# Optimization experiments

Measured on AMD Instinct MI355X. Metric: run time of the kernel, lower is better.

## Reference

```python
import jax, jax.numpy as jnp
import numpy as np

EPS = 1e-5

def conv3d(x, w, b):
    y = jax.lax.conv_general_dilated(x, w, (1, 1, 1), [(1, 1), (1, 1), (1, 1)],
                                     dimension_numbers=('NCDHW', 'OIDHW', 'NCDHW'))
    return y + b[None, :, None, None, None]

def batchnorm(x, g, b):
    # training-mode BN: biased batch statistics over (N, D, H, W)
    m = jnp.mean(x, axis=(0, 2, 3, 4), keepdims=True)
    v = jnp.mean((x - m) ** 2, axis=(0, 2, 3, 4), keepdims=True)
    return (x - m) * jax.lax.rsqrt(v + EPS) * g[None, :, None, None, None] + b[None, :, None, None, None]

def deform_conv3d(x, offset, w, b):
    # x: (B,C,D,H,W); offset: (B, 3*27, D,H,W); w: (O,C,3,3,3)
    B, C, D, H, W = x.shape
    N = 27
    xp = jnp.pad(x, ((0, 0), (0, 0), (1, 1), (1, 1), (1, 1)))
    Dp, Hp, Wp = D + 2, H + 2, W + 2
    off = offset.reshape(B, 3, N, D, H, W)
    kk = jnp.arange(3, dtype=x.dtype) - 1.0  # kernel taps -1,0,1
    kd, kh, kw = [a.reshape(-1) for a in jnp.meshgrid(kk, kk, kk, indexing='ij')]
    # sampling positions in padded coords: p0 (=out idx + pad) + kernel tap + learned offset
    pd = jnp.clip((jnp.arange(D, dtype=x.dtype) + 1.0)[None, None, :, None, None]
                  + kd[None, :, None, None, None] + off[:, 0], 0.0, Dp - 1)
    ph = jnp.clip((jnp.arange(H, dtype=x.dtype) + 1.0)[None, None, None, :, None]
                  + kh[None, :, None, None, None] + off[:, 1], 0.0, Hp - 1)
    pw = jnp.clip((jnp.arange(W, dtype=x.dtype) + 1.0)[None, None, None, None, :]
                  + kw[None, :, None, None, None] + off[:, 2], 0.0, Wp - 1)
    q0d = jnp.clip(jnp.floor(pd), 0, Dp - 2); td = jnp.clip(pd - q0d, 0.0, 1.0)
    q0h = jnp.clip(jnp.floor(ph), 0, Hp - 2); th = jnp.clip(ph - q0h, 0.0, 1.0)
    q0w = jnp.clip(jnp.floor(pw), 0, Wp - 2); tw = jnp.clip(pw - q0w, 0.0, 1.0)
    q0d = q0d.astype(jnp.int32); q0h = q0h.astype(jnp.int32); q0w = q0w.astype(jnp.int32)
    xf = xp.reshape(B, C, -1)
    acc = jnp.zeros((B, C, N, D, H, W), dtype=x.dtype)
    for i in (0, 1):
        for j in (0, 1):
            for k in (0, 1):
                idx = ((q0d + i) * Hp + (q0h + j)) * Wp + (q0w + k)  # (B,N,D,H,W)
                g = ((td if i else 1.0 - td) * (th if j else 1.0 - th) * (tw if k else 1.0 - tw))
                gath = jnp.take_along_axis(xf, idx.reshape(B, 1, -1), axis=2).reshape(B, C, N, D, H, W)
                acc = acc + g[:, None] * gath
    out = jnp.einsum('bcndhw,ocn->bodhw', acc, w.reshape(w.shape[0], C, N))
    return out + b[None, :, None, None, None]


def setup_inputs() -> dict:
    ks = jax.random.split(jax.random.key(0), 16)
    s = 0.05
    f32 = jnp.float32
    return {
        'x': jax.random.normal(ks[0], (4, 1, 28, 28, 8), f32),
        'c1w': jax.random.normal(ks[1], (32, 1, 3, 3, 3), f32) * s, 'c1b': jnp.zeros((32,), f32),
        'g1': jnp.ones((32,), f32), 'b1': jnp.zeros((32,), f32),
        'c2w': jax.random.normal(ks[2], (64, 32, 3, 3, 3), f32) * s, 'c2b': jnp.zeros((64,), f32),
        'g2': jnp.ones((64,), f32), 'b2': jnp.zeros((64,), f32),
        'c3w': jax.random.normal(ks[3], (128, 64, 3, 3, 3), f32) * s, 'c3b': jnp.zeros((128,), f32),
        'g3': jnp.ones((128,), f32), 'b3': jnp.zeros((128,), f32),
        'ow': jax.random.normal(ks[4], (81, 128, 3, 3, 3), f32) * s, 'ob': jnp.zeros((81,), f32),
        'dw': jax.random.normal(ks[5], (128, 128, 3, 3, 3), f32) * s, 'db': jnp.zeros((128,), f32),
        'g4': jnp.ones((128,), f32), 'b4': jnp.zeros((128,), f32),
        'fcw': jax.random.normal(ks[6], (10, 128), f32) * s, 'fcb': jnp.zeros((10,), f32),
    }


def reference(x, c1w, c1b, g1, b1, c2w, c2b, g2, b2, c3w, c3b, g3, b3,
              ow, ob, dw, db, g4, b4, fcw, fcb):
    h = batchnorm(jax.nn.relu(conv3d(x, c1w, c1b)), g1, b1)
    h = batchnorm(jax.nn.relu(conv3d(h, c2w, c2b)), g2, b2)
    h = batchnorm(jax.nn.relu(conv3d(h, c3w, c3b)), g3, b3)
    offsets = conv3d(h, ow, ob)
    h = batchnorm(jax.nn.relu(deform_conv3d(h, offsets, dw, db)), g4, b4)
    pooled = jnp.mean(h, axis=(2, 3, 4))  # avg_pool over full (28,28,d) extent
    logits = pooled @ fcw.T + fcb
    return jax.nn.log_softmax(logits, axis=1), offsets
```

## Files before the change

kernel.cpp:

```cpp
#include <hip/hip_runtime.h>
#include <hip/hip_bf16.h>
#include <math.h>

#define BB 4
#define SP 6272
#define NSP 25088
#define EPS 1e-5f

typedef unsigned short u16;
typedef __attribute__((ext_vector_type(8))) short v8s;
typedef __attribute__((ext_vector_type(4))) float v4f;

__device__ __forceinline__ u16 f2b(float f) {
    unsigned u = __float_as_uint(f);
    return (u16)((u + 0x7fffu + ((u >> 16) & 1u)) >> 16);
}
__device__ __forceinline__ float b2f(u16 s) {
    return __uint_as_float(((unsigned)s) << 16);
}
__device__ __forceinline__ float b2f_lo(unsigned x) { return __uint_as_float(x << 16); }
__device__ __forceinline__ float b2f_hi(unsigned x) { return __uint_as_float(x & 0xffff0000u); }
__device__ __forceinline__ unsigned pk2(float a, float b) {
    __hip_bfloat162 h = __float22bfloat162_rn(make_float2(a, b));
    unsigned u;
    __builtin_memcpy(&u, &h, 4);
    return u;
}

__global__ __launch_bounds__(256) __attribute__((amdgpu_waves_per_eu(1, 4)))
void conv1_shfl(const float* __restrict__ X, const float* __restrict__ Wt,
                const float* __restrict__ bias, u16* __restrict__ Ybf,
                float* __restrict__ s_sum, float* __restrict__ s_sq)
{
    const int OT = 16;
    __shared__ float red[4][32];
    int xblk = blockIdx.x;
    int sblk = (xblk & 7) * 13 + (xblk >> 3);
    if (sblk >= 98) return;
    int t = threadIdx.x;
    int s = sblk * 256 + t;
    int b = s / SP;
    int sp = s - b * SP;
    int d = sp / 224;
    int r = sp - d * 224;
    int h = r >> 3;
    int w = r & 7;
    int o0 = blockIdx.y * OT;

    float mdh[9]; int odh[9];
    #pragma unroll
    for (int i = 0; i < 3; i++) {
        int dd = d + i - 1;
        float md = ((unsigned)dd < 28u) ? 1.f : 0.f;
        int ddc = min(max(dd, 0), 27);
        #pragma unroll
        for (int j = 0; j < 3; j++) {
            int hh = h + j - 1;
            float mh = ((unsigned)hh < 28u) ? 1.f : 0.f;
            int hhc = min(max(hh, 0), 27);
            mdh[i * 3 + j] = md * mh;
            odh[i * 3 + j] = ddc * 224 + hhc * 8 + w;
        }
    }
    float mw0 = (w > 0) ? 1.f : 0.f;
    float mw2 = (w < 7) ? 1.f : 0.f;

    float acc[OT];
    #pragma unroll
    for (int oo = 0; oo < OT; oo++) acc[oo] = bias[o0 + oo];

    const float* xc = X + (size_t)b * SP;
    #pragma unroll
    for (int t9 = 0; t9 < 9; t9++) {
        float x0 = xc[odh[t9]];
        float m = mdh[t9];
        float xm = __shfl_up(x0, 1, 64) * (m * mw0);
        float xz = x0 * m;
        float xp = __shfl_down(x0, 1, 64) * (m * mw2);
        #pragma unroll
        for (int oo = 0; oo < OT; oo++) {
            const float* wp = Wt + (size_t)(o0 + oo) * 27 + t9 * 3;
            acc[oo] = fmaf(xm, wp[0], acc[oo]);
            acc[oo] = fmaf(xz, wp[1], acc[oo]);
            acc[oo] = fmaf(xp, wp[2], acc[oo]);
        }
    }
    float sv[OT];
    #pragma unroll
    for (int oo = 0; oo < OT; oo++) sv[oo] = fmaxf(acc[oo], 0.f);

    unsigned pk[8];
    #pragma unroll
    for (int j = 0; j < 8; j++) pk[j] = pk2(sv[2 * j], sv[2 * j + 1]);
    u16* row = Ybf + (size_t)(b * SP + sp) * 32 + o0;
    *(uint4*)(row)     = make_uint4(pk[0], pk[1], pk[2], pk[3]);
    *(uint4*)(row + 8) = make_uint4(pk[4], pk[5], pk[6], pk[7]);

    int l = t & 63, wvv = t >> 6;
    #pragma unroll
    for (int oo = 0; oo < OT; oo++) {
        float ss = sv[oo], qv = ss * ss;
        #pragma unroll
        for (int m = 1; m < 64; m <<= 1) {
            ss += __shfl_xor(ss, m, 64);
            qv += __shfl_xor(qv, m, 64);
        }
        if (l == 0) { red[wvv][oo] = ss; red[wvv][16 + oo] = qv; }
    }
    __syncthreads();
    if (t < 32) {
        float tot = red[0][t] + red[1][t] + red[2][t] + red[3][t];
        if (t < 16) atomicAdd(&s_sum[o0 + t], tot);
        else        atomicAdd(&s_sq[o0 + t - 16], tot);
    }
}

__global__ __launch_bounds__(256) void prepack_all(const float* __restrict__ c2w,
        const float* __restrict__ c3w, const float* __restrict__ ow,
        const float* __restrict__ dw, u16* __restrict__ wpk2,
        u16* __restrict__ wpk3, u16* __restrict__ wpko, u16* __restrict__ dwa,
        float* __restrict__ ws0)
{
    int bx = blockIdx.x;
    if (bx >= 4536) {
        int i = (bx - 4536) * 256 + threadIdx.x;
        if (i < 2048) ws0[i] = 0.f;
        return;
    }
    int idx = bx * 256 + threadIdx.x;
    if (idx < 55296) {
        int i = idx;
        int j = i & 7, r = (i >> 3) & 15, q = (i >> 7) & 3;
        int ot = (i >> 9) & 3, t = i >> 11;
        int o = ot * 16 + r, c = q * 8 + j;
        wpk2[i] = f2b(c2w[((size_t)o * 32 + c) * 27 + t]);
    } else if (idx < 276480) {
        int i = idx - 55296;
        int j = i & 7, r = (i >> 3) & 15, q = (i >> 7) & 3;
        int ch = (i >> 9) & 1, ot = (i >> 10) & 7, t = i >> 13;
        int o = ot * 16 + r, c = ch * 32 + q * 8 + j;
        wpk3[i] = f2b(c3w[((size_t)o * 64 + c) * 27 + t]);
    } else if (idx < 718848) {
        int i = idx - 276480;
        int j = i & 7, r = (i >> 3) & 15, q = (i >> 7) & 3;
        int ch = (i >> 9) & 3, ot = (i >> 11) & 7, t = i >> 14;
        int o = ot * 16 + r, c = ch * 32 + q * 8 + j;
        wpko[i] = f2b((o < 81) ? ow[((size_t)o * 128 + c) * 27 + t] : 0.f);
    } else {
        int i = idx - 718848;
        int j = i & 7, r = (i >> 3) & 15, q = (i >> 7) & 3;
        int kc = (i >> 9) & 3, ot = (i >> 11) & 7, n = i >> 14;
        int o = ot * 16 + r, c = kc * 32 + q * 8 + j;
        dwa[i] = f2b(dw[((size_t)o * 128 + c) * 27 + n]);
    }
}

template<int CIN, int OPAD, bool OFFOUT, bool BNIN, bool WIDE>
__global__ __launch_bounds__(256) __attribute__((amdgpu_waves_per_eu(1, 4)))
void conv_mfma(const u16* __restrict__ X, const u16* __restrict__ Wpk,
               const float* __restrict__ bias, u16* __restrict__ Ybf,
               float* __restrict__ offs, float* __restrict__ s_sum,
               float* __restrict__ s_sq, const float* __restrict__ in_sum,
               const float* __restrict__ in_sq, const float* __restrict__ in_g,
               const float* __restrict__ in_b)
{
    const int HS = CIN + 8;
    const int NOT = OPAD / 16;
    const int NC = CIN / 32;
    __shared__ u16 xs[160 * HS];
    __shared__ float scin[BNIN ? CIN : 1], shin[BNIN ? CIN : 1];

    int tid = threadIdx.x;
    int fid = blockIdx.x;
    int g = (fid & 7) * 98 + (fid >> 3);
    int b = g / 196;
    int rem = g - b * 196;
    int d0 = (rem / 14) * 2, h0 = (rem % 14) * 2;

    if (BNIN) {
        if (tid < CIN) {
            float m = in_sum[tid] * (1.f / NSP);
            float v = in_sq[tid] * (1.f / NSP) - m * m;
            float sc = in_g[tid] * rsqrtf(v + EPS);
            scin[tid] = sc;
            shin[tid] = in_b[tid] - m * sc;
        }
        __syncthreads();
    }

    const int NCH = CIN / 8;
    for (int idx = tid; idx < 160 * NCH; idx += 256) {
        int pos = idx / NCH, ch = idx - pos * NCH;
        int dz = pos / 40, r2 = pos - dz * 40;
        int hz = r2 / 10, wz = r2 - hz * 10;
        int dd = d0 + dz - 1, hh = h0 + hz - 1, ww = wz - 1;
        uint4 val = make_uint4(0, 0, 0, 0);
        if ((unsigned)dd < 28u && (unsigned)hh < 28u && (unsigned)ww < 8u) {
            val = *(const uint4*)(X + ((size_t)(b * SP + dd * 224 + hh * 8 + ww) * CIN + ch * 8));
            if (BNIN) {
                int cb = ch * 8;
                float f0 = b2f_lo(val.x) * scin[cb]     + shin[cb];
                float f1 = b2f_hi(val.x) * scin[cb + 1] + shin[cb + 1];
                float f2 = b2f_lo(val.y) * scin[cb + 2] + shin[cb + 2];
                float f3 = b2f_hi(val.y) * scin[cb + 3] + shin[cb + 3];
                float f4 = b2f_lo(val.z) * scin[cb + 4] + shin[cb + 4];
                float f5 = b2f_hi(val.z) * scin[cb + 5] + shin[cb + 5];
                float f6 = b2f_lo(val.w) * scin[cb + 6] + shin[cb + 6];
                float f7 = b2f_hi(val.w) * scin[cb + 7] + shin[cb + 7];
                val.x = pk2(f0, f1); val.y = pk2(f2, f3);
                val.z = pk2(f4, f5); val.w = pk2(f6, f7);
            }
        }
        *(uint4*)(xs + pos * HS + ch * 8) = val;
    }
    __syncthreads();

    int l = tid & 63, wv = tid >> 6;
    int q = l >> 4, r = l & 15;
    int hl = r >> 3, wl = r & 7;

    if (OFFOUT) {
        int dl = wv >> 1;
        int ot0 = (wv & 1) * 3;
        const u16* ap = xs + ((4 + hl + 1) * 10 + wl + 1) * HS + 8 * q + dl * 40 * HS;
        v4f acc[3];
        acc[0] = (v4f){0.f,0.f,0.f,0.f};
        acc[1] = (v4f){0.f,0.f,0.f,0.f};
        acc[2] = (v4f){0.f,0.f,0.f,0.f};
        #pragma unroll
        for (int t = 0; t < 27; t++) {
            const int koff = ((t / 9) - 1) * 40 + (((t / 3) % 3) - 1) * 10 + (t % 3) - 1;
            const u16* wt = Wpk + ((size_t)(t * NOT + ot0) * NC << 9) + l * 8;
            #pragma unroll
            for (int ch = 0; ch < NC; ch++) {
                v8s a0 = *(const v8s*)(ap + koff * HS + ch * 32);
                v8s b0 = *(const v8s*)(wt + ch * 512);
                v8s b1 = *(const v8s*)(wt + (NC + ch) * 512);
                v8s b2 = *(const v8s*)(wt + (2 * NC + ch) * 512);
                acc[0] = __builtin_amdgcn_mfma_f32_16x16x32_bf16(a0, b0, acc[0], 0, 0, 0);
                acc[1] = __builtin_amdgcn_mfma_f32_16x16x32_bf16(a0, b1, acc[1], 0, 0, 0);
// ... 54 lines not shown
                for (int rg = 0; rg < 4; rg++) {
                    int rowl = q * 4 + rg;
                    int sp = (d0 + s2) * 224 + (h0 + (rowl >> 3)) * 8 + (rowl & 7);
                    float v = fmaxf(A[rg] + bo, 0.f);
                    Ybf[(size_t)(b * SP + sp) * OPAD + oo] = f2b(v);
                    rs += v; rq += v * v;
                }
            }
            rs += __shfl_xor(rs, 16, 64); rs += __shfl_xor(rs, 32, 64);
            rq += __shfl_xor(rq, 16, 64); rq += __shfl_xor(rq, 32, 64);
            if (l < 16) { atomicAdd(&s_sum[o_base + l], rs); atomicAdd(&s_sq[o_base + l], rq); }
        }
        return;
    }

    int o_base = blockIdx.y * 64 + wv * 16;
    int o = o_base + r;
    int otg = o_base >> 4;

    v4f acc0 = {0.f, 0.f, 0.f, 0.f}, acc1 = {0.f, 0.f, 0.f, 0.f};
    #pragma unroll
    for (int t = 0; t < 27; t++) {
        const int koff = ((t / 9) - 1) * 40 + (((t / 3) % 3) - 1) * 10 + (t % 3) - 1;
        const u16* wt = Wpk + ((size_t)(t * NOT + otg) * NC << 9) + l * 8;
        #pragma unroll
        for (int ch = 0; ch < NC; ch++) {
            v8s a0 = *(const v8s*)(a0p + koff * HS + ch * 32);
            v8s a1 = *(const v8s*)(a1p + koff * HS + ch * 32);
            v8s bf = *(const v8s*)(wt + ch * 512);
            acc0 = __builtin_amdgcn_mfma_f32_16x16x32_bf16(a0, bf, acc0, 0, 0, 0);
            acc1 = __builtin_amdgcn_mfma_f32_16x16x32_bf16(a1, bf, acc1, 0, 0, 0);
        }
    }

    {
        float bo = bias[o];
        float rs = 0.f, rq = 0.f;
        #pragma unroll
        for (int s2 = 0; s2 < 2; s2++) {
            v4f A = s2 ? acc1 : acc0;
            #pragma unroll
            for (int rg = 0; rg < 4; rg++) {
                int rowl = q * 4 + rg;
                int sp = (d0 + s2) * 224 + (h0 + (rowl >> 3)) * 8 + (rowl & 7);
                float v = fmaxf(A[rg] + bo, 0.f);
                Ybf[(size_t)(b * SP + sp) * OPAD + o] = f2b(v);
                rs += v; rq += v * v;
            }
        }
        rs += __shfl_xor(rs, 16, 64); rs += __shfl_xor(rs, 32, 64);
        rq += __shfl_xor(rq, 16, 64); rq += __shfl_xor(rq, 32, 64);
        if (l < 16) { atomicAdd(&s_sum[o_base + l], rs); atomicAdd(&s_sq[o_base + l], rq); }
    }
}

template<int C>
__global__ __launch_bounds__(256) void bn_bf(const u16* __restrict__ Y,
        const float* __restrict__ s_sum, const float* __restrict__ s_sq,
        const float* __restrict__ g, const float* __restrict__ bb,
        u16* __restrict__ Xo)
{
    __shared__ float sc_s[C], sh_s[C];
    int t = threadIdx.x;
    if (t < C) {
        float m  = s_sum[t] * (1.f / NSP);
        float v  = s_sq[t] * (1.f / NSP) - m * m;
        float sc = g[t] * rsqrtf(v + EPS);
        sc_s[t] = sc;
        sh_s[t] = bb[t] - m * sc;
    }
    __syncthreads();
    int idx = blockIdx.x * 256 + t;
    uint4 v = ((const uint4*)Y)[idx];
    int cb = (idx & (C / 8 - 1)) * 8;
    float f0 = b2f_lo(v.x) * sc_s[cb]     + sh_s[cb];
    float f1 = b2f_hi(v.x) * sc_s[cb + 1] + sh_s[cb + 1];
    float f2 = b2f_lo(v.y) * sc_s[cb + 2] + sh_s[cb + 2];
    float f3 = b2f_hi(v.y) * sc_s[cb + 3] + sh_s[cb + 3];
    float f4 = b2f_lo(v.z) * sc_s[cb + 4] + sh_s[cb + 4];
    float f5 = b2f_hi(v.z) * sc_s[cb + 5] + sh_s[cb + 5];
    float f6 = b2f_lo(v.w) * sc_s[cb + 6] + sh_s[cb + 6];
    float f7 = b2f_hi(v.w) * sc_s[cb + 7] + sh_s[cb + 7];
    uint4 pk;
    pk.x = pk2(f0, f1); pk.y = pk2(f2, f3);
    pk.z = pk2(f4, f5); pk.w = pk2(f6, f7);
    ((uint4*)Xo)[idx] = pk;
}

__global__ __launch_bounds__(256) __attribute__((amdgpu_waves_per_eu(1, 4)))
void deform_pool(const u16* __restrict__ Ht, const float* __restrict__ OFF,
                 const u16* __restrict__ Wa, const float* __restrict__ db,
                 float* __restrict__ pooledraw, float* __restrict__ sumsq4)
{
    __shared__ float offs_lds[81 * 32];
    __shared__ int ig_s[2][32][8][2];
    __shared__ u16 Vb[2][32][136];
    __shared__ float reds[128], redq[128];

    int fid = blockIdx.x;
    int xcd = fid & 7;
    int local = fid >> 3;
    if (local >= 98) return;
    int b = xcd >> 1;
    int d = (xcd & 1) * 14 + local / 7;
    int h0 = (local % 7) * 4;

    int t = threadIdx.x;
    if (t < 128) { reds[t] = 0.f; redq[t] = 0.f; }

    int gp = t >> 3, gcr = t & 7;
    int glh = gp >> 3, gw = gp & 7, gh = h0 + glh;
    int co = t & 15, pg = t >> 4;
    int l = t & 63, wv = t >> 6;
    int q = l >> 4, r = l & 15;

    v4f acc[2][2];
    acc[0][0] = (v4f){0.f,0.f,0.f,0.f}; acc[0][1] = (v4f){0.f,0.f,0.f,0.f};
    acc[1][0] = (v4f){0.f,0.f,0.f,0.f}; acc[1][1] = (v4f){0.f,0.f,0.f,0.f};

    const u16* hb = Ht + (size_t)b * SP * 128;

    for (int i = t; i < 2592; i += 256) {
        int ch = i >> 5, p = i & 31;
        offs_lds[i] = OFF[(size_t)b * 81 * SP + (size_t)ch * SP
                          + d * 224 + (h0 + (p >> 3)) * 8 + (p & 7)];
    }

    auto GEOM = [&](int n, int tap) {
        int kd = n / 9 - 1, kh = (n / 3) % 3 - 1, kw = n % 3 - 1;
        float od  = offs_lds[n * 32 + gp];
        float oh  = offs_lds[(27 + n) * 32 + gp];
        float owv = offs_lds[(54 + n) * 32 + gp];
        float pd = fminf(fmaxf((float)(d + 1 + kd) + od, 0.f), 29.f);
        float ph = fminf(fmaxf((float)(gh + 1 + kh) + oh, 0.f), 29.f);
        float pw = fminf(fmaxf((float)(gw + 1 + kw) + owv, 0.f), 9.f);
        float qd = fminf(floorf(pd), 28.f);
        float qh = fminf(floorf(ph), 28.f);
        float qw = fminf(floorf(pw), 8.f);
        float td = fminf(pd - qd, 1.f);
        float th = fminf(ph - qh, 1.f);
        float tw = fminf(pw - qw, 1.f);
        int iqd = (int)qd - 1, iqh = (int)qh - 1, iqw = (int)qw - 1;
        int i = gcr >> 2, j = (gcr >> 1) & 1, k = gcr & 1;
        int du = iqd + i, hu = iqh + j, wu = iqw + k;
        bool val = (unsigned)du < 28u && (unsigned)hu < 28u && (unsigned)wu < 8u;
        float gg = (i ? td : 1.f - td) * (j ? th : 1.f - th) * (k ? tw : 1.f - tw);
        ig_s[tap][gp][gcr][0] = val ? (du * 224 + hu * 8 + wu) : 0;
        ig_s[tap][gp][gcr][1] = __float_as_int(val ? gg : 0.f);
    };

    auto SAMPLE = [&](int tap) {
        #pragma unroll
        for (int pp = 0; pp < 2; pp++) {
            int p = pg * 2 + pp;
            float va[8] = {0.f,0.f,0.f,0.f,0.f,0.f,0.f,0.f};
            #pragma unroll
            for (int cr = 0; cr < 8; cr++) {
                int2 pr = *(const int2*)&ig_s[tap][p][cr][0];
                float gg = __int_as_float(pr.y);
                uint4 xv = *(const uint4*)(hb + (size_t)pr.x * 128 + co * 8);
                va[0] = fmaf(gg, b2f_lo(xv.x), va[0]);
                va[1] = fmaf(gg, b2f_hi(xv.x), va[1]);
                va[2] = fmaf(gg, b2f_lo(xv.y), va[2]);
                va[3] = fmaf(gg, b2f_hi(xv.y), va[3]);
                va[4] = fmaf(gg, b2f_lo(xv.z), va[4]);
                va[5] = fmaf(gg, b2f_hi(xv.z), va[5]);
                va[6] = fmaf(gg, b2f_lo(xv.w), va[6]);
                va[7] = fmaf(gg, b2f_hi(xv.w), va[7]);
            }
            uint4 pk;
            pk.x = pk2(va[0], va[1]); pk.y = pk2(va[2], va[3]);
            pk.z = pk2(va[4], va[5]); pk.w = pk2(va[6], va[7]);
            *(uint4*)&Vb[tap][p][co * 8] = pk;
        }
    };

    auto MFMA_TAP = [&](int n, int tap) {
        const u16* wn = Wa + (size_t)n * 16384;
        #pragma unroll
        for (int oti = 0; oti < 2; oti++) {
            int ot = wv * 2 + oti;
            #pragma unroll
            for (int kc = 0; kc < 4; kc++) {
                v8s af = *(const v8s*)(wn + ((((ot * 4 + kc) * 4 + q) * 16 + r) * 8));
                v8s bf0 = *(const v8s*)&Vb[tap][r][kc * 32 + q * 8];
                v8s bf1 = *(const v8s*)&Vb[tap][16 + r][kc * 32 + q * 8];
                acc[oti][0] = __builtin_amdgcn_mfma_f32_16x16x32_bf16(af, bf0, acc[oti][0], 0, 0, 0);
                acc[oti][1] = __builtin_amdgcn_mfma_f32_16x16x32_bf16(af, bf1, acc[oti][1], 0, 0, 0);
            }
        }
    };

    for (int it = 0; it < 14; it++) {
        int n0 = it * 2, n1 = n0 + 1;
        bool two = (n1 < 27);
        __syncthreads();
        GEOM(n0, 0);
        if (two) GEOM(n1, 1);
        __syncthreads();
        SAMPLE(0);
        if (two) SAMPLE(1);
        __syncthreads();
        MFMA_TAP(n0, 0);
        if (two) MFMA_TAP(n1, 1);
    }

    #pragma unroll
    for (int oti = 0; oti < 2; oti++) {
        #pragma unroll
        for (int rg = 0; rg < 4; rg++) {
            int o = (wv * 2 + oti) * 16 + q * 4 + rg;
            float bo = db[o];
            float v0 = fmaxf(acc[oti][0][rg] + bo, 0.f);
            float v1 = fmaxf(acc[oti][1][rg] + bo, 0.f);
            float s = v0 + v1, qq = v0 * v0 + v1 * v1;
            s += __shfl_xor(s, 1, 64);  qq += __shfl_xor(qq, 1, 64);
            s += __shfl_xor(s, 2, 64);  qq += __shfl_xor(qq, 2, 64);
            s += __shfl_xor(s, 4, 64);  qq += __shfl_xor(qq, 4, 64);
            s += __shfl_xor(s, 8, 64);  qq += __shfl_xor(qq, 8, 64);
            if (r == 0) { atomicAdd(&reds[o], s); atomicAdd(&redq[o], qq); }
        }
    }
    __syncthreads();
    if (t < 128) {
        atomicAdd(&pooledraw[b * 128 + t], reds[t]);
        atomicAdd(&sumsq4[t], redq[t]);
    }
}

__global__ __launch_bounds__(256) void final_head_emit(const float* __restrict__ pooledraw,
        const float* __restrict__ sumsq4, const float* __restrict__ g4,
        const float* __restrict__ b4, const float* __restrict__ fcw,
        const float* __restrict__ fcb, float* __restrict__ out)
{
    int t = threadIdx.x;
    __shared__ float pooled_s[4][128];
    __shared__ float logits[4][10];
    if (t < 128) {
        float s0 = pooledraw[t], s1 = pooledraw[128 + t];
        float s2 = pooledraw[256 + t], s3 = pooledraw[384 + t];
        float tot = s0 + s1 + s2 + s3;
        float m  = tot * (1.f / NSP);
        float v  = sumsq4[t] * (1.f / NSP) - m * m;
        float sc = g4[t] * rsqrtf(v + EPS);
        float sh = b4[t] - m * sc;
        pooled_s[0][t] = s0 * (1.f / SP) * sc + sh;
        pooled_s[1][t] = s1 * (1.f / SP) * sc + sh;
        pooled_s[2][t] = s2 * (1.f / SP) * sc + sh;
        pooled_s[3][t] = s3 * (1.f / SP) * sc + sh;
    }
    __syncthreads();
    if (t < 40) {
        int b = t / 10, j = t % 10;
        float l = fcb[j];
        for (int c = 0; c < 128; c++) l = fmaf(pooled_s[b][c], fcw[j * 128 + c], l);
        logits[b][j] = l;
    }
    __syncthreads();
    if (t < 4) {
        float mx = -1e30f;
        for (int j = 0; j < 10; j++) mx = fmaxf(mx, logits[t][j]);
        float se = 0.f;
        for (int j = 0; j < 10; j++) se += expf(logits[t][j] - mx);
        float lse = mx + logf(se);
        for (int j = 0; j < 10; j++) out[t * 10 + j] = logits[t][j] - lse;
    }
}

extern "C" void kernel_launch(void* const* d_in, const int* in_sizes, int n_in,
                              void* d_out, int out_size, void* d_ws, size_t ws_size,
                              hipStream_t stream)
{
    (void)in_sizes; (void)n_in; (void)out_size; (void)ws_size;
    const float* x   = (const float*)d_in[0];
    const float* c1w = (const float*)d_in[1];
    const float* c1b = (const float*)d_in[2];
    const float* g1  = (const float*)d_in[3];
    const float* b1  = (const float*)d_in[4];
    const float* c2w = (const float*)d_in[5];
    const float* c2b = (const float*)d_in[6];
    const float* g2  = (const float*)d_in[7];
    const float* b2  = (const float*)d_in[8];
    const float* c3w = (const float*)d_in[9];
    const float* c3b = (const float*)d_in[10];
    const float* g3  = (const float*)d_in[11];
    const float* b3  = (const float*)d_in[12];
    const float* ow  = (const float*)d_in[13];
    const float* ob  = (const float*)d_in[14];
    const float* dw  = (const float*)d_in[15];
    const float* db  = (const float*)d_in[16];
    const float* g4  = (const float*)d_in[17];
    const float* b4  = (const float*)d_in[18];
    const float* fcw = (const float*)d_in[19];
    const float* fcb = (const float*)d_in[20];

    float* ws = (float*)d_ws;
    float* S1 = ws + 0,   *Q1 = ws + 32;
    float* S2 = ws + 64,  *Q2 = ws + 128;
    float* S3 = ws + 192, *Q3 = ws + 320;
    float* PO = ws + 448;
    float* Q4 = ws + 960;
    u16* y1bf = (u16*)(ws + 2048);
    u16* y2bf = y1bf + 802816;
    u16* y3bf = y2bf + 1605632;
    u16* x3bf = y3bf + 3211264;
    u16* wpk2 = x3bf + 3211264;
    u16* wpk3 = wpk2 + 55296;
    u16* wpko = wpk3 + 221184;
    u16* dwa  = wpko + 442368;

    float* outf = (float*)d_out;
    float* offp = outf + 40;

    prepack_all<<<4544, 256, 0, stream>>>(c2w, c3w, ow, dw, wpk2, wpk3, wpko, dwa, ws);

    conv1_shfl<<<dim3(104, 2), 256, 0, stream>>>(x, c1w, c1b, y1bf, S1, Q1);

    conv_mfma<32, 64, false, true, false><<<dim3(784, 1), 256, 0, stream>>>(
        y1bf, wpk2, c2b, y2bf, nullptr, S2, Q2, S1, Q1, g1, b1);

    conv_mfma<64, 128, false, true, true><<<dim3(784, 1), 256, 0, stream>>>(
        y2bf, wpk3, c3b, y3bf, nullptr, S3, Q3, S2, Q2, g2, b2);

    bn_bf<128><<<1568, 256, 0, stream>>>(y3bf, S3, Q3, g3, b3, x3bf);

    conv_mfma<128, 128, true, false, false><<<dim3(784, 1), 256, 0, stream>>>(
        x3bf, wpko, ob, nullptr, offp, nullptr, nullptr, nullptr, nullptr, nullptr, nullptr);

    deform_pool<<<800, 256, 0, stream>>>(x3bf, offp, dwa, db, PO, Q4);
    final_head_emit<<<1, 256, 0, stream>>>(PO, Q4, g4, b4, fcw, fcb, outf);
}
```

Measured before the change: 339.6 us.

## Fuse final head into deform_pool via last-block counter; batch gather loads

Folds the final BN/FC/log-softmax kernel into deform_pool. Each block bumps a global atomic counter, and the last block to finish reads the accumulated sums and computes the head, which removes one kernel launch. It also restructures SAMPLE to issue all eight gather loads before the FMAs and to use packed float2 math, aiming for more memory-level parallelism. The counter at ws+1100 must be zeroed before each call (possibly in prepack, not visible here), and the restructuring adds register pressure.

```diff
diff --git a/kernel.cpp b/kernel.cpp
--- a/kernel.cpp
+++ b/kernel.cpp
@@ -10,6 +10,7 @@
 typedef unsigned short u16;
 typedef __attribute__((ext_vector_type(8))) short v8s;
 typedef __attribute__((ext_vector_type(4))) float v4f;
+typedef __attribute__((ext_vector_type(2))) float f32x2;
 
 __device__ __forceinline__ u16 f2b(float f) {
     unsigned u = __float_as_uint(f);
@@ -384,180 +385,199 @@
 __global__ __launch_bounds__(256) __attribute__((amdgpu_waves_per_eu(1, 4)))
 void deform_pool(const u16* __restrict__ Ht, const float* __restrict__ OFF,
                  const u16* __restrict__ Wa, const float* __restrict__ db,
-                 float* __restrict__ pooledraw, float* __restrict__ sumsq4)
+                 float* __restrict__ pooledraw, float* __restrict__ sumsq4,
+                 unsigned* __restrict__ cnt, const float* __restrict__ g4,
+                 const float* __restrict__ b4, const float* __restrict__ fcw,
+                 const float* __restrict__ fcb, float* __restrict__ out)
 {
     __shared__ float offs_lds[81 * 32];
     __shared__ int ig_s[2][32][8][2];
     __shared__ u16 Vb[2][32][136];
     __shared__ float reds[128], redq[128];
+    __shared__ unsigned done_s;
 
     int fid = blockIdx.x;
     int xcd = fid & 7;
     int local = fid >> 3;
-    if (local >= 98) return;
-    int b = xcd >> 1;
-    int d = (xcd & 1) * 14 + local / 7;
-    int h0 = (local % 7) * 4;
-
     int t = threadIdx.x;
-    if (t < 128) { reds[t] = 0.f; redq[t] = 0.f; }
-
-    int gp = t >> 3, gcr = t & 7;
-    int glh = gp >> 3, gw = gp & 7, gh = h0 + glh;
-    int co = t & 15, pg = t >> 4;
-    int l = t & 63, wv = t >> 6;
-    int q = l >> 4, r = l & 15;
-
-    v4f acc[2][2];
-    acc[0][0] = (v4f){0.f,0.f,0.f,0.f}; acc[0][1] = (v4f){0.f,0.f,0.f,0.f};
-    acc[1][0] = (v4f){0.f,0.f,0.f,0.f}; acc[1][1] = (v4f){0.f,0.f,0.f,0.f};
-
-    const u16* hb = Ht + (size_t)b * SP * 128;
-
-    for (int i = t; i < 2592; i += 256) {
-        int ch = i >> 5, p = i & 31;
-        offs_lds[i] = OFF[(size_t)b * 81 * SP + (size_t)ch * SP
-                          + d * 224 + (h0 + (p >> 3)) * 8 + (p & 7)];
-    }
-
-    auto GEOM = [&](int n, int tap) {
-        int kd = n / 9 - 1, kh = (n / 3) % 3 - 1, kw = n % 3 - 1;
-        float od  = offs_lds[n * 32 + gp];
-        float oh  = offs_lds[(27 + n) * 32 + gp];
-        float owv = offs_lds[(54 + n) * 32 + gp];
-        float pd = fminf(fmaxf((float)(d + 1 + kd) + od, 0.f), 29.f);
-        float ph = fminf(fmaxf((float)(gh + 1 + kh) + oh, 0.f), 29.f);
-        float pw = fminf(fmaxf((float)(gw + 1 + kw) + owv, 0.f), 9.f);
-        float qd = fminf(floorf(pd), 28.f);
-        float qh = fminf(floorf(ph), 28.f);
-        float qw = fminf(floorf(pw), 8.f);
-        float td = fminf(pd - qd, 1.f);
-        float th = fminf(ph - qh, 1.f);
-        float tw = fminf(pw - qw, 1.f);
-        int iqd = (int)qd - 1, iqh = (int)qh - 1, iqw = (int)qw - 1;
-        int i = gcr >> 2, j = (gcr >> 1) & 1, k = gcr & 1;
-        int du = iqd + i, hu = iqh + j, wu = iqw + k;
-        bool val = (unsigned)du < 28u && (unsigned)hu < 28u && (unsigned)wu < 8u;
-        float gg = (i ? td : 1.f - td) * (j ? th : 1.f - th) * (k ? tw : 1.f - tw);
-        ig_s[tap][gp][gcr][0] = val ? (du * 224 + hu * 8 + wu) : 0;
-        ig_s[tap][gp][gcr][1] = __float_as_int(val ? gg : 0.f);
-    };
-
-    auto SAMPLE = [&](int tap) {
-        #pragma unroll
-        for (int pp = 0; pp < 2; pp++) {
-            int p = pg * 2 + pp;
-            float va[8] = {0.f,0.f,0.f,0.f,0.f,0.f,0.f,0.f};
+
+    if (local < 98) {
+        int b = xcd >> 1;
+        int d = (xcd & 1) * 14 + local / 7;
+        int h0 = (local % 7) * 4;
+
+        if (t < 128) { reds[t] = 0.f; redq[t] = 0.f; }
+
+        int gp = t >> 3, gcr = t & 7;
+        int glh = gp >> 3, gw = gp & 7, gh = h0 + glh;
+        int co = t & 15, pg = t >> 4;
+        int l = t & 63, wv = t >> 6;
+        int q = l >> 4, r = l & 15;
+
+        v4f acc[2][2];
+        acc[0][0] = (v4f){0.f,0.f,0.f,0.f}; acc[0][1] = (v4f){0.f,0.f,0.f,0.f};
+        acc[1][0] = (v4f){0.f,0.f,0.f,0.f}; acc[1][1] = (v4f){0.f,0.f,0.f,0.f};
+
+        const u16* hb = Ht + (size_t)b * SP * 128;
+
+        for (int i = t; i < 2592; i += 256) {
+            int ch = i >> 5, p = i & 31;
+            offs_lds[i] = OFF[(size_t)b * 81 * SP + (size_t)ch * SP
+                              + d * 224 + (h0 + (p >> 3)) * 8 + (p & 7)];
+        }
+
+        auto GEOM = [&](int n, int tap) {
+            int kd = n / 9 - 1, kh = (n / 3) % 3 - 1, kw = n % 3 - 1;
+            float od  = offs_lds[n * 32 + gp];
+            float oh  = offs_lds[(27 + n) * 32 + gp];
+            float owv = offs_lds[(54 + n) * 32 + gp];
+            float pd = fminf(fmaxf((float)(d + 1 + kd) + od, 0.f), 29.f);
+            float ph = fminf(fmaxf((float)(gh + 1 + kh) + oh, 0.f), 29.f);
+            float pw = fminf(fmaxf((float)(gw + 1 + kw) + owv, 0.f), 9.f);
+            float qd = fminf(floorf(pd), 28.f);
+            float qh = fminf(floorf(ph), 28.f);
+            float qw = fminf(floorf(pw), 8.f);
+            float td = fminf(pd - qd, 1.f);
+            float th = fminf(ph - qh, 1.f);
+            float tw = fminf(pw - qw, 1.f);
+            int iqd = (int)qd - 1, iqh = (int)qh - 1, iqw = (int)qw - 1;
+            int i = gcr >> 2, j = (gcr >> 1) & 1, k = gcr & 1;
+            int du = iqd + i, hu = iqh + j, wu = iqw + k;
+            bool val = (unsigned)du < 28u && (unsigned)hu < 28u && (unsigned)wu < 8u;
+            float gg = (i ? td : 1.f - td) * (j ? th : 1.f - th) * (k ? tw : 1.f - tw);
+            ig_s[tap][gp][gcr][0] = val ? (du * 224 + hu * 8 + wu) : 0;
+            ig_s[tap][gp][gcr][1] = __float_as_int(val ? gg : 0.f);
+        };
+
+        auto SAMPLE = [&](int tap) {
             #pragma unroll
-            for (int cr = 0; cr < 8; cr++) {
-                int2 pr = *(const int2*)&ig_s[tap][p][cr][0];
-                float gg = __int_as_float(pr.y);
-                uint4 xv = *(const uint4*)(hb + (size_t)pr.x * 128 + co * 8);
-                va[0] = fmaf(gg, b2f_lo(xv.x), va[0]);
-                va[1] = fmaf(gg, b2f_hi(xv.x), va[1]);
-                va[2] = fmaf(gg, b2f_lo(xv.y), va[2]);
-                va[3] = fmaf(gg, b2f_hi(xv.y), va[3]);
-                va[4] = fmaf(gg, b2f_lo(xv.z), va[4]);
-                va[5] = fmaf(gg, b2f_hi(xv.z), va[5]);
-                va[6] = fmaf(gg, b2f_lo(xv.w), va[6]);
-                va[7] = fmaf(gg, b2f_hi(xv.w), va[7]);
-            }
-            uint4 pk;
-            pk.x = pk2(va[0], va[1]); pk.y = pk2(va[2], va[3]);
-            pk.z = pk2(va[4], va[5]); pk.w = pk2(va[6], va[7]);
-            *(uint4*)&Vb[tap][p][co * 8] = pk;
-        }
-    };
-
-    auto MFMA_TAP = [&](int n, int tap) {
-        const u16* wn = Wa + (size_t)n * 16384;
+            for (int pp = 0; pp < 2; pp++) {
+                int p = pg * 2 + pp;
+                int2 prs[8];
+                #pragma unroll
+                for (int cr = 0; cr < 8; cr++)
+                    prs[cr] = *(const int2*)&ig_s[tap][p][cr][0];
+                uint4 xv[8];
+                #pragma unroll
+                for (int cr = 0; cr < 8; cr++)
+                    xv[cr] = *(const uint4*)(hb + (size_t)prs[cr].x * 128 + co * 8);
+                f32x2 va2[4];
+                va2[0] = (f32x2){0.f, 0.f}; va2[1] = (f32x2){0.f, 0.f};
+                va2[2] = (f32x2){0.f, 0.f}; va2[3] = (f32x2){0.f, 0.f};
+                #pragma unroll
+                for (int cr = 0; cr < 8; cr++) {
+                    float gg = __int_as_float(prs[cr].y);
+                    f32x2 g2 = {gg, gg};
+                    f32x2 x0 = { b2f_lo(xv[cr].x), b2f_hi(xv[cr].x) };
+                    f32x2 x1 = { b2f_lo(xv[cr].y), b2f_hi(xv[cr].y) };
+                    f32x2 x2 = { b2f_lo(xv[cr].z), b2f_hi(xv[cr].z) };
+                    f32x2 x3 = { b2f_lo(xv[cr].w), b2f_hi(xv[cr].w) };
+                    va2[0] = g2 * x0 + va2[0];
+                    va2[1] = g2 * x1 + va2[1];
+                    va2[2] = g2 * x2 + va2[2];
+                    va2[3] = g2 * x3 + va2[3];
+                }
+                uint4 pk;
+                pk.x = pk2(va2[0].x, va2[0].y); pk.y = pk2(va2[1].x, va2[1].y);
+                pk.z = pk2(va2[2].x, va2[2].y); pk.w = pk2(va2[3].x, va2[3].y);
+                *(uint4*)&Vb[tap][p][co * 8] = pk;
+            }
+        };
+
+        auto MFMA_TAP = [&](int n, int tap) {
+            const u16* wn = Wa + (size_t)n * 16384;
+            #pragma unroll
+            for (int oti = 0; oti < 2; oti++) {
+                int ot = wv * 2 + oti;
+                #pragma unroll
+                for (int kc = 0; kc < 4; kc++) {
+                    v8s af = *(const v8s*)(wn + ((((ot * 4 + kc) * 4 + q) * 16 + r) * 8));
+                    v8s bf0 = *(const v8s*)&Vb[tap][r][kc * 32 + q * 8];
+                    v8s bf1 = *(const v8s*)&Vb[tap][16 + r][kc * 32 + q * 8];
+                    acc[oti][0] = __builtin_amdgcn_mfma_f32_16x16x32_bf16(af, bf0, acc[oti][0], 0, 0, 0);
+                    acc[oti][1] = __builtin_amdgcn_mfma_f32_16x16x32_bf16(af, bf1, acc[oti][1], 0, 0, 0);
+                }
+            }
+        };
+
+        for (int it = 0; it < 14; it++) {
+            int n0 = it * 2, n1 = n0 + 1;
+            bool two = (n1 < 27);
+            __syncthreads();
+            GEOM(n0, 0);
+            if (two) GEOM(n1, 1);
+            __syncthreads();
+            SAMPLE(0);
+            if (two) SAMPLE(1);
+            __syncthreads();
+            MFMA_TAP(n0, 0);
+            if (two) MFMA_TAP(n1, 1);
+        }
+
         #pragma unroll
         for (int oti = 0; oti < 2; oti++) {
-            int ot = wv * 2 + oti;
             #pragma unroll
-            for (int kc = 0; kc < 4; kc++) {
-                v8s af = *(const v8s*)(wn + ((((ot * 4 + kc) * 4 + q) * 16 + r) * 8));
-                v8s bf0 = *(const v8s*)&Vb[tap][r][kc * 32 + q * 8];
-                v8s bf1 = *(const v8s*)&Vb[tap][16 + r][kc * 32 + q * 8];
-                acc[oti][0] = __builtin_amdgcn_mfma_f32_16x16x32_bf16(af, bf0, acc[oti][0], 0, 0, 0);
-                acc[oti][1] = __builtin_amdgcn_mfma_f32_16x16x32_bf16(af, bf1, acc[oti][1], 0, 0, 0);
-            }
-        }
-    };
-
-    for (int it = 0; it < 14; it++) {
-        int n0 = it * 2, n1 = n0 + 1;
-        bool two = (n1 < 27);
+            for (int rg = 0; rg < 4; rg++) {
+                int o = (wv * 2 + oti) * 16 + q * 4 + rg;
+                float bo = db[o];
+                float v0 = fmaxf(acc[oti][0][rg] + bo, 0.f);
+                float v1 = fmaxf(acc[oti][1][rg] + bo, 0.f);
+                float s = v0 + v1, qq = v0 * v0 + v1 * v1;
+                s += __shfl_xor(s, 1, 64);  qq += __shfl_xor(qq, 1, 64);
+                s += __shfl_xor(s, 2, 64);  qq += __shfl_xor(qq, 2, 64);
+                s += __shfl_xor(s, 4, 64);  qq += __shfl_xor(qq, 4, 64);
+                s += __shfl_xor(s, 8, 64);  qq += __shfl_xor(qq, 8, 64);
+                if (r == 0) { atomicAdd(&reds[o], s); atomicAdd(&redq[o], qq); }
+            }
+        }
         __syncthreads();
-        GEOM(n0, 0);
-        if (two) GEOM(n1, 1);
+        if (t < 128) {
+            atomicAdd(&pooledraw[b * 128 + t], reds[t]);
+            atomicAdd(&sumsq4[t], redq[t]);
+        }
+    }
+
+    __syncthreads();
+    if (t == 0) {
+        __threadfence();
+        done_s = atomicAdd(cnt, 1u);
+    }
+    __syncthreads();
+    if (done_s == 799u) {
+        __shared__ float pooled_s[4][128];
+        __shared__ float logits_s[4][10];
+        if (t < 128) {
+            float s0 = __hip_atomic_load(&pooledraw[t],       __ATOMIC_RELAXED, __HIP_MEMORY_SCOPE_AGENT);
+            float s1 = __hip_atomic_load(&pooledraw[128 + t], __ATOMIC_RELAXED, __HIP_MEMORY_SCOPE_AGENT);
+            float s2 = __hip_atomic_load(&pooledraw[256 + t], __ATOMIC_RELAXED, __HIP_MEMORY_SCOPE_AGENT);
+            float s3 = __hip_atomic_load(&pooledraw[384 + t], __ATOMIC_RELAXED, __HIP_MEMORY_SCOPE_AGENT);
+            float qv = __hip_atomic_load(&sumsq4[t],          __ATOMIC_RELAXED, __HIP_MEMORY_SCOPE_AGENT);
+            float tot = s0 + s1 + s2 + s3;
+            float m  = tot * (1.f / NSP);
+            float v  = qv * (1.f / NSP) - m * m;
+            float sc = g4[t] * rsqrtf(v + EPS);
+            float sh = b4[t] - m * sc;
+            pooled_s[0][t] = s0 * (1.f / SP) * sc + sh;
+            pooled_s[1][t] = s1 * (1.f / SP) * sc + sh;
+            pooled_s[2][t] = s2 * (1.f / SP) * sc + sh;
+            pooled_s[3][t] = s3 * (1.f / SP) * sc + sh;
+        }
         __syncthreads();
-        SAMPLE(0);
-        if (two) SAMPLE(1);
+        if (t < 40) {
+            int b = t / 10, j = t % 10;
+            float lg = fcb[j];
+            for (int c = 0; c < 128; c++) lg = fmaf(pooled_s[b][c], fcw[j * 128 + c], lg);
+            logits_s[b][j] = lg;
+        }
         __syncthreads();
-        MFMA_TAP(n0, 0);
-        if (two) MFMA_TAP(n1, 1);
-    }
-
-    #pragma unroll
-    for (int oti = 0; oti < 2; oti++) {
-        #pragma unroll
-        for (int rg = 0; rg < 4; rg++) {
-            int o = (wv * 2 + oti) * 16 + q * 4 + rg;
-            float bo = db[o];
-            float v0 = fmaxf(acc[oti][0][rg] + bo, 0.f);
-            float v1 = fmaxf(acc[oti][1][rg] + bo, 0.f);
-            float s = v0 + v1, qq = v0 * v0 + v1 * v1;
-            s += __shfl_xor(s, 1, 64);  qq += __shfl_xor(qq, 1, 64);
-            s += __shfl_xor(s, 2, 64);  qq += __shfl_xor(qq, 2, 64);
-            s += __shfl_xor(s, 4, 64);  qq += __shfl_xor(qq, 4, 64);
-            s += __shfl_xor(s, 8, 64);  qq += __shfl_xor(qq, 8, 64);
-            if (r == 0) { atomicAdd(&reds[o], s); atomicAdd(&redq[o], qq); }
-        }
-    }
-    __syncthreads();
-    if (t < 128) {
-        atomicAdd(&pooledraw[b * 128 + t], reds[t]);
-        atomicAdd(&sumsq4[t], redq[t]);
-    }
-}
-
-__global__ __launch_bounds__(256) void final_head_emit(const float* __restrict__ pooledraw,
-        const float* __restrict__ sumsq4, const float* __restrict__ g4,
-        const float* __restrict__ b4, const float* __restrict__ fcw,
-        const float* __restrict__ fcb, float* __restrict__ out)
-{
-    int t = threadIdx.x;
-    __shared__ float pooled_s[4][128];
-    __shared__ float logits[4][10];
-    if (t < 128) {
-        float s0 = pooledraw[t], s1 = pooledraw[128 + t];
-        float s2 = pooledraw[256 + t], s3 = pooledraw[384 + t];
-        float tot = s0 + s1 + s2 + s3;
-        float m  = tot * (1.f / NSP);
-        float v  = sumsq4[t] * (1.f / NSP) - m * m;
-        float sc = g4[t] * rsqrtf(v + EPS);
-        float sh = b4[t] - m * sc;
-        pooled_s[0][t] = s0 * (1.f / SP) * sc + sh;
-        pooled_s[1][t] = s1 * (1.f / SP) * sc + sh;
-        pooled_s[2][t] = s2 * (1.f / SP) * sc + sh;
-        pooled_s[3][t] = s3 * (1.f / SP) * sc + sh;
-    }
-    __syncthreads();
-    if (t < 40) {
-        int b = t / 10, j = t % 10;
-        float l = fcb[j];
-        for (int c = 0; c < 128; c++) l = fmaf(pooled_s[b][c], fcw[j * 128 + c], l);
-        logits[b][j] = l;
-    }
-    __syncthreads();
-    if (t < 4) {
-        float mx = -1e30f;
-        for (int j = 0; j < 10; j++) mx = fmaxf(mx, logits[t][j]);
-        float se = 0.f;
-        for (int j = 0; j < 10; j++) se += expf(logits[t][j] - mx);
-        float lse = mx + logf(se);
-        for (int j = 0; j < 10; j++) out[t * 10 + j] = logits[t][j] - lse;
+        if (t < 4) {
+            float mx = -1e30f;
+            for (int j = 0; j < 10; j++) mx = fmaxf(mx, logits_s[t][j]);
+            float se = 0.f;
+            for (int j = 0; j < 10; j++) se += expf(logits_s[t][j] - mx);
+            float lse = mx + logf(se);
+            for (int j = 0; j < 10; j++) out[t * 10 + j] = logits_s[t][j] - lse;
+        }
     }
 }
 
@@ -594,6 +614,7 @@
     float* S3 = ws + 192, *Q3 = ws + 320;
     float* PO = ws + 448;
     float* Q4 = ws + 960;
+    unsigned* cnt = (unsigned*)(ws + 1100);
     u16* y1bf = (u16*)(ws + 2048);
     u16* y2bf = y1bf + 802816;
     u16* y3bf = y2bf + 1605632;
@@ -621,6 +642,6 @@
     conv_mfma<128, 128, true, false, false><<<dim3(784, 1), 256, 0, stream>>>(
         x3bf, wpko, ob, nullptr, offp, nullptr, nullptr, nullptr, nullptr, nullptr, nullptr);
 
-    deform_pool<<<800, 256, 0, stream>>>(x3bf, offp, dwa, db, PO, Q4);
-    final_head_emit<<<1, 256, 0, stream>>>(PO, Q4, g4, b4, fcw, fcb, outf);
-}
+    deform_pool<<<800, 256, 0, stream>>>(x3bf, offp, dwa, db, PO, Q4, cnt,
+                                         g4, b4, fcw, fcb, outf);
+}
```

New measurement: 343.2 us. No clear change (+1.0%).

## Fuse conv1 into prepack launch and BN3 into offset-conv input path

Applied to the files above, without the earlier changes.

Moves the conv1 computation into the prepack kernel as extra blocks and replaces its atomics with per-block partial sums, which conv2 reduces at startup. The offset conv now applies BN3 on the fly from the raw conv3 output, and extra blocks of the same launch write the normalized x3 buffer for the deform stage. Two kernel launches are removed, cutting launch overhead and one pass over memory, at the cost of redundant per-block stat reductions and mixed-role grids.

```diff
diff --git a/kernel.cpp b/kernel.cpp
--- a/kernel.cpp
+++ b/kernel.cpp
@@ -27,107 +27,109 @@
     return u;
 }
 
-__global__ __launch_bounds__(256) __attribute__((amdgpu_waves_per_eu(1, 4)))
-void conv1_shfl(const float* __restrict__ X, const float* __restrict__ Wt,
-                const float* __restrict__ bias, u16* __restrict__ Ybf,
-                float* __restrict__ s_sum, float* __restrict__ s_sq)
-{
-    const int OT = 16;
-    __shared__ float red[4][32];
-    int xblk = blockIdx.x;
-    int sblk = (xblk & 7) * 13 + (xblk >> 3);
-    if (sblk >= 98) return;
-    int t = threadIdx.x;
-    int s = sblk * 256 + t;
-    int b = s / SP;
-    int sp = s - b * SP;
-    int d = sp / 224;
-    int r = sp - d * 224;
-    int h = r >> 3;
-    int w = r & 7;
-    int o0 = blockIdx.y * OT;
-
-    float mdh[9]; int odh[9];
-    #pragma unroll
-    for (int i = 0; i < 3; i++) {
-        int dd = d + i - 1;
-        float md = ((unsigned)dd < 28u) ? 1.f : 0.f;
-        int ddc = min(max(dd, 0), 27);
-        #pragma unroll
-        for (int j = 0; j < 3; j++) {
-            int hh = h + j - 1;
-            float mh = ((unsigned)hh < 28u) ? 1.f : 0.f;
-            int hhc = min(max(hh, 0), 27);
-            mdh[i * 3 + j] = md * mh;
-            odh[i * 3 + j] = ddc * 224 + hhc * 8 + w;
-        }
-    }
-    float mw0 = (w > 0) ? 1.f : 0.f;
-    float mw2 = (w < 7) ? 1.f : 0.f;
-
-    float acc[OT];
-    #pragma unroll
-    for (int oo = 0; oo < OT; oo++) acc[oo] = bias[o0 + oo];
-
-    const float* xc = X + (size_t)b * SP;
-    #pragma unroll
-    for (int t9 = 0; t9 < 9; t9++) {
-        float x0 = xc[odh[t9]];
-        float m = mdh[t9];
-        float xm = __shfl_up(x0, 1, 64) * (m * mw0);
-        float xz = x0 * m;
-        float xp = __shfl_down(x0, 1, 64) * (m * mw2);
-        #pragma unroll
-        for (int oo = 0; oo < OT; oo++) {
-            const float* wp = Wt + (size_t)(o0 + oo) * 27 + t9 * 3;
-            acc[oo] = fmaf(xm, wp[0], acc[oo]);
-            acc[oo] = fmaf(xz, wp[1], acc[oo]);
-            acc[oo] = fmaf(xp, wp[2], acc[oo]);
-        }
-    }
-    float sv[OT];
-    #pragma unroll
-    for (int oo = 0; oo < OT; oo++) sv[oo] = fmaxf(acc[oo], 0.f);
-
-    unsigned pk[8];
-    #pragma unroll
-    for (int j = 0; j < 8; j++) pk[j] = pk2(sv[2 * j], sv[2 * j + 1]);
-    u16* row = Ybf + (size_t)(b * SP + sp) * 32 + o0;
-    *(uint4*)(row)     = make_uint4(pk[0], pk[1], pk[2], pk[3]);
-    *(uint4*)(row + 8) = make_uint4(pk[4], pk[5], pk[6], pk[7]);
-
-    int l = t & 63, wvv = t >> 6;
-    #pragma unroll
-    for (int oo = 0; oo < OT; oo++) {
-        float ss = sv[oo], qv = ss * ss;
-        #pragma unroll
-        for (int m = 1; m < 64; m <<= 1) {
-            ss += __shfl_xor(ss, m, 64);
-            qv += __shfl_xor(qv, m, 64);
-        }
-        if (l == 0) { red[wvv][oo] = ss; red[wvv][16 + oo] = qv; }
-    }
-    __syncthreads();
-    if (t < 32) {
-        float tot = red[0][t] + red[1][t] + red[2][t] + red[3][t];
-        if (t < 16) atomicAdd(&s_sum[o0 + t], tot);
-        else        atomicAdd(&s_sq[o0 + t - 16], tot);
-    }
-}
-
 __global__ __launch_bounds__(256) void prepack_all(const float* __restrict__ c2w,
         const float* __restrict__ c3w, const float* __restrict__ ow,
         const float* __restrict__ dw, u16* __restrict__ wpk2,
         u16* __restrict__ wpk3, u16* __restrict__ wpko, u16* __restrict__ dwa,
-        float* __restrict__ ws0)
+        float* __restrict__ ws0, const float* __restrict__ X,
+        const float* __restrict__ Wt, const float* __restrict__ c1b,
+        u16* __restrict__ Ybf, float* __restrict__ P1s, float* __restrict__ P1q)
 {
     int bx = blockIdx.x;
+    int tid = threadIdx.x;
+
+    if (bx >= 4544) {
+        const int OT = 16;
+        __shared__ float red[4][32];
+        int c = bx - 4544;
+        int xblk = c % 104;
+        int o0 = (c / 104) * OT;
+        int sblk = (xblk & 7) * 13 + (xblk >> 3);
+        if (sblk >= 98) return;
+        int t = tid;
+        int s = sblk * 256 + t;
+        int b = s / SP;
+        int sp = s - b * SP;
+        int d = sp / 224;
+        int r = sp - d * 224;
+        int h = r >> 3;
+        int w = r & 7;
+
+        float mdh[9]; int odh[9];
+        #pragma unroll
+        for (int i = 0; i < 3; i++) {
+            int dd = d + i - 1;
+            float md = ((unsigned)dd < 28u) ? 1.f : 0.f;
+            int ddc = min(max(dd, 0), 27);
+            #pragma unroll
+            for (int j = 0; j < 3; j++) {
+                int hh = h + j - 1;
+                float mh = ((unsigned)hh < 28u) ? 1.f : 0.f;
+                int hhc = min(max(hh, 0), 27);
+                mdh[i * 3 + j] = md * mh;
+                odh[i * 3 + j] = ddc * 224 + hhc * 8 + w;
+            }
+        }
+        float mw0 = (w > 0) ? 1.f : 0.f;
+        float mw2 = (w < 7) ? 1.f : 0.f;
+
+        float acc[OT];
+        #pragma unroll
+        for (int oo = 0; oo < OT; oo++) acc[oo] = c1b[o0 + oo];
+
+        const float* xc = X + (size_t)b * SP;
+        #pragma unroll
+        for (int t9 = 0; t9 < 9; t9++) {
+            float x0 = xc[odh[t9]];
+            float m = mdh[t9];
+            float xm = __shfl_up(x0, 1, 64) * (m * mw0);
+            float xz = x0 * m;
+            float xp = __shfl_down(x0, 1, 64) * (m * mw2);
+            #pragma unroll
+            for (int oo = 0; oo < OT; oo++) {
+                const float* wp = Wt + (size_t)(o0 + oo) * 27 + t9 * 3;
+                acc[oo] = fmaf(xm, wp[0], acc[oo]);
+                acc[oo] = fmaf(xz, wp[1], acc[oo]);
+                acc[oo] = fmaf(xp, wp[2], acc[oo]);
+            }
+        }
+        float sv[OT];
+        #pragma unroll
+        for (int oo = 0; oo < OT; oo++) sv[oo] = fmaxf(acc[oo], 0.f);
+
+        unsigned pk[8];
+        #pragma unroll
+        for (int j = 0; j < 8; j++) pk[j] = pk2(sv[2 * j], sv[2 * j + 1]);
+        u16* row = Ybf + (size_t)(b * SP + sp) * 32 + o0;
+        *(uint4*)(row)     = make_uint4(pk[0], pk[1], pk[2], pk[3]);
+        *(uint4*)(row + 8) = make_uint4(pk[4], pk[5], pk[6], pk[7]);
+
+        int l = t & 63, wvv = t >> 6;
+        #pragma unroll
+        for (int oo = 0; oo < OT; oo++) {
+            float ss = sv[oo], qv = ss * ss;
+            #pragma unroll
+            for (int m = 1; m < 64; m <<= 1) {
+                ss += __shfl_xor(ss, m, 64);
+                qv += __shfl_xor(qv, m, 64);
+            }
+            if (l == 0) { red[wvv][oo] = ss; red[wvv][16 + oo] = qv; }
+        }
+        __syncthreads();
+        if (t < 32) {
+            float tot = red[0][t] + red[1][t] + red[2][t] + red[3][t];
+            if (t < 16) P1s[sblk * 32 + o0 + t] = tot;
+            else        P1q[sblk * 32 + o0 + (t - 16)] = tot;
+        }
+        return;
+    }
+
     if (bx >= 4536) {
-        int i = (bx - 4536) * 256 + threadIdx.x;
+        int i = (bx - 4536) * 256 + tid;
         if (i < 2048) ws0[i] = 0.f;
         return;
     }
-    int idx = bx * 256 + threadIdx.x;
+    int idx = bx * 256 + tid;
     if (idx < 55296) {
         int i = idx;
         int j = i & 7, r = (i >> 3) & 15, q = (i >> 7) & 3;
@@ -155,7 +157,7 @@
     }
 }
 
-template<int CIN, int OPAD, bool OFFOUT, bool BNIN, bool WIDE>
+template<int CIN, int OPAD, bool OFFOUT, bool BNIN, bool WIDE, bool PARTIN, bool BNTAIL>
 __global__ __launch_bounds__(256) __attribute__((amdgpu_waves_per_eu(1, 4)))
 void conv_mfma(const u16* __restrict__ X, const u16* __restrict__ Wpk,
                const float* __restrict__ bias, u16* __restrict__ Ybf,
@@ -178,14 +180,56 @@
     int d0 = (rem / 14) * 2, h0 = (rem % 14) * 2;
 
     if (BNIN) {
-        if (tid < CIN) {
-            float m = in_sum[tid] * (1.f / NSP);
-            float v = in_sq[tid] * (1.f / NSP) - m * m;
-            float sc = in_g[tid] * rsqrtf(v + EPS);
-            scin[tid] = sc;
-            shin[tid] = in_b[tid] - m * sc;
-        }
-        __syncthreads();
+        if (PARTIN) {
+            __shared__ float ps[8][32], pq[8][32];
+            int ch = tid & 31, ck = tid >> 5;
+            float s = 0.f, qq = 0.f;
+            for (int k = ck; k < 98; k += 8) {
+                s  += in_sum[k * 32 + ch];
+                qq += in_sq[k * 32 + ch];
+            }
+            ps[ck][ch] = s; pq[ck][ch] = qq;
+            __syncthreads();
+            if (tid < CIN) {
+                float m = 0.f, vq = 0.f;
+                #pragma unroll
+                for (int k2 = 0; k2 < 8; k2++) { m += ps[k2][tid]; vq += pq[k2][tid]; }
+                m *= (1.f / NSP);
+                vq = vq * (1.f / NSP) - m * m;
+                float sc = in_g[tid] * rsqrtf(vq + EPS);
+                scin[tid] = sc;
+                shin[tid] = in_b[tid] - m * sc;
+            }
+            __syncthreads();
+        } else {
+            if (tid < CIN) {
+                float m = in_sum[tid] * (1.f / NSP);
+                float v = in_sq[tid] * (1.f / NSP) - m * m;
+                float sc = in_g[tid] * rsqrtf(v + EPS);
+                scin[tid] = sc;
+                shin[tid] = in_b[tid] - m * sc;
+            }
+            __syncthreads();
+        }
+    }
+
+    if (BNTAIL && fid >= 784) {
+        int idx = (fid - 784) * 256 + tid;
+        uint4 v = ((const uint4*)X)[idx];
+        int cb = (idx & (CIN / 8 - 1)) * 8;
+        float f0 = b2f_lo(v.x) * scin[cb]     + shin[cb];
+        float f1 = b2f_hi(v.x) * scin[cb + 1] + shin[cb + 1];
+        float f2 = b2f_lo(v.y) * scin[cb + 2] + shin[cb + 2];
+        float f3 = b2f_hi(v.y) * scin[cb + 3] + shin[cb + 3];
+        float f4 = b2f_lo(v.z) * scin[cb + 4] + shin[cb + 4];
+        float f5 = b2f_hi(v.z) * scin[cb + 5] + shin[cb + 5];
+        float f6 = b2f_lo(v.w) * scin[cb + 6] + shin[cb + 6];
+        float f7 = b2f_hi(v.w) * scin[cb + 7] + shin[cb + 7];
+        uint4 pk;
+        pk.x = pk2(f0, f1); pk.y = pk2(f2, f3);
+        pk.z = pk2(f4, f5); pk.w = pk2(f6, f7);
+        ((uint4*)Ybf)[idx] = pk;
+        return;
     }
 
     const int NCH = CIN / 8;
@@ -346,39 +390,6 @@
         rq += __shfl_xor(rq, 16, 64); rq += __shfl_xor(rq, 32, 64);
         if (l < 16) { atomicAdd(&s_sum[o_base + l], rs); atomicAdd(&s_sq[o_base + l], rq); }
     }
-}
-
-template<int C>
-__global__ __launch_bounds__(256) void bn_bf(const u16* __restrict__ Y,
-        const float* __restrict__ s_sum, const float* __restrict__ s_sq,
-        const float* __restrict__ g, const float* __restrict__ bb,
-        u16* __restrict__ Xo)
-{
-    __shared__ float sc_s[C], sh_s[C];
-    int t = threadIdx.x;
-    if (t < C) {
-        float m  = s_sum[t] * (1.f / NSP);
-        float v  = s_sq[t] * (1.f / NSP) - m * m;
-        float sc = g[t] * rsqrtf(v + EPS);
-        sc_s[t] = sc;
-        sh_s[t] = bb[t] - m * sc;
-    }
-    __syncthreads();
-    int idx = blockIdx.x * 256 + t;
-    uint4 v = ((const uint4*)Y)[idx];
-    int cb = (idx & (C / 8 - 1)) * 8;
-    float f0 = b2f_lo(v.x) * sc_s[cb]     + sh_s[cb];
-    float f1 = b2f_hi(v.x) * sc_s[cb + 1] + sh_s[cb + 1];
-    float f2 = b2f_lo(v.y) * sc_s[cb + 2] + sh_s[cb + 2];
-    float f3 = b2f_hi(v.y) * sc_s[cb + 3] + sh_s[cb + 3];
-    float f4 = b2f_lo(v.z) * sc_s[cb + 4] + sh_s[cb + 4];
-    float f5 = b2f_hi(v.z) * sc_s[cb + 5] + sh_s[cb + 5];
-    float f6 = b2f_lo(v.w) * sc_s[cb + 6] + sh_s[cb + 6];
-    float f7 = b2f_hi(v.w) * sc_s[cb + 7] + sh_s[cb + 7];
-    uint4 pk;
-    pk.x = pk2(f0, f1); pk.y = pk2(f2, f3);
-    pk.z = pk2(f4, f5); pk.w = pk2(f6, f7);
-    ((uint4*)Xo)[idx] = pk;
 }
 
 __global__ __launch_bounds__(256) __attribute__((amdgpu_waves_per_eu(1, 4)))
@@ -589,12 +600,13 @@
     const float* fcb = (const float*)d_in[20];
 
     float* ws = (float*)d_ws;
-    float* S1 = ws + 0,   *Q1 = ws + 32;
     float* S2 = ws + 64,  *Q2 = ws + 128;
     float* S3 = ws + 192, *Q3 = ws + 320;
     float* PO = ws + 448;
     float* Q4 = ws + 960;
-    u16* y1bf = (u16*)(ws + 2048);
+    float* P1s = ws + 4096;
+    float* P1q = ws + 7232;
+    u16* y1bf = (u16*)(ws + 16384);
     u16* y2bf = y1bf + 802816;
     u16* y3bf = y2bf + 1605632;
     u16* x3bf = y3bf + 3211264;
@@ -606,21 +618,19 @@
     float* outf = (float*)d_out;
     float* offp = outf + 40;
 
-    prepack_all<<<4544, 256, 0, stream>>>(c2w, c3w, ow, dw, wpk2, wpk3, wpko, dwa, ws);
-
-    conv1_shfl<<<dim3(104, 2), 256, 0, stream>>>(x, c1w, c1b, y1bf, S1, Q1);
-
-    conv_mfma<32, 64, false, true, false><<<dim3(784, 1), 256, 0, stream>>>(
-        y1bf, wpk2, c2b, y2bf, nullptr, S2, Q2, S1, Q1, g1, b1);
-
-    conv_mfma<64, 128, false, true, true><<<dim3(784, 1), 256, 0, stream>>>(
+    prepack_all<<<4752, 256, 0, stream>>>(c2w, c3w, ow, dw, wpk2, wpk3, wpko, dwa,
+                                          ws, x, c1w, c1b, y1bf, P1s, P1q);
+
+    conv_mfma<32, 64, false, true, false, true, false><<<784, 256, 0, stream>>>(
+        y1bf, wpk2, c2b, y2bf, nullptr, S2, Q2, P1s, P1q, g1, b1);
+
+    conv_mfma<64, 128, false, true, true, false, false><<<784, 256, 0, stream>>>(
         y2bf, wpk3, c3b, y3bf, nullptr, S3, Q3, S2, Q2, g2, b2);
 
-    bn_bf<128><<<1568, 256, 0, stream>>>(y3bf, S3, Q3, g3, b3, x3bf);
-
-    conv_mfma<128, 128, true, false, false><<<dim3(784, 1), 256, 0, stream>>>(
-        x3bf, wpko, ob, nullptr, offp, nullptr, nullptr, nullptr, nullptr, nullptr, nullptr);
+    conv_mfma<128, 128, true, true, false, false, true><<<2352, 256, 0, stream>>>(
+        y3bf, wpko, ob, x3bf, offp, nullptr, nullptr, S3, Q3, g3, b3);
 
     deform_pool<<<800, 256, 0, stream>>>(x3bf, offp, dwa, db, PO, Q4);
+
     final_head_emit<<<1, 256, 0, stream>>>(PO, Q4, g4, b4, fcw, fcb, outf);
 }
```

Result: no change. 341.8 us (+0.6%).
